# Performance work log

Hardware: AMD Instinct MI355X
Metric: run time of the kernel (lower is better)

The kernel has to match this reference:

```python
import jax, jax.numpy as jnp
import numpy as np

B, T, D = 4096, 200, 64
H = 32  # hidden units of score MLP
NEG_INF = jnp.float32(-2**32 + 1)


def setup_inputs() -> dict:
    key = jax.random.key(0)
    k1, k2, k3, k4, k5 = jax.random.split(key, 5)
    query = jax.random.normal(k1, (B, 1, D), dtype=jnp.float32)
    keys = jax.random.normal(k2, (B, T, D), dtype=jnp.float32)
    mask = jax.random.randint(k3, (B, T), 0, 2) > 0
    mask = mask.at[:, 0].set(True)  # ensure at least one valid key per row
    # Glorot-normal-ish init for the tiny score MLP
    W1 = jax.random.normal(k4, (3 * D, H), dtype=jnp.float32) * jnp.sqrt(2.0 / (3 * D + H))
    b1 = jnp.zeros((H,), dtype=jnp.float32)
    W2 = jax.random.normal(k5, (H, 1), dtype=jnp.float32) * jnp.sqrt(2.0 / (H + 1))
    b2 = jnp.zeros((1,), dtype=jnp.float32)
    return {"query": query, "keys": keys, "mask": mask,
            "W1": W1, "b1": b1, "W2": W2, "b2": b2}


def reference(query, keys, mask, W1, b1, W2, b2):
    b, t, d = keys.shape
    q = jnp.broadcast_to(query, (b, t, d))            # tile query over seq
    att_in = jnp.concatenate([q, keys, q - keys], axis=-1)   # [B,T,3D]
    h = jax.nn.sigmoid(att_in @ W1 + b1)              # [B,T,H]
    score = (h @ W2 + b2)[..., 0]                     # [B,T]
    score = jnp.where(mask, score, NEG_INF)
    w = jax.nn.softmax(score, axis=-1)                # [B,T]
    out = jnp.einsum('bt,btd->bd', w, keys)           # weighted key sum
    return out[:, None, :]                            # [B,1,D]
```

## Files before the change

kernel.cpp:

```cpp
#include <hip/hip_runtime.h>
#include <hip/hip_bf16.h>


#define B 4096
#define T 200
#define D 64
#define H 32
#define LOG2E 1.44269504088896340736f
#define SOFF 16.0f
#define NTILE 13

typedef __attribute__((ext_vector_type(8))) short short8;
typedef __attribute__((ext_vector_type(4))) float f32x4;


__global__ __launch_bounds__(256) void prep_kernel(
        const float* __restrict__ W1,
        const float* __restrict__ b1,
        const float* __restrict__ query,
        float*       __restrict__ ws)
{
    int blk = blockIdx.x;
    int tid = threadIdx.x;
    if (blk < 512) {
        int n = blk * 256 + tid;
        int b = n >> 5;
        int j = n & 31;
        const float* qb = query + (size_t)b * D;
        float acc = b1[j];
        #pragma unroll 8
        for (int i = 0; i < D; ++i)
            acc = fmaf(qb[i], W1[i * H + j] + W1[(128 + i) * H + j], acc);
        ws[n] = acc;
    } else {
        int m = (blk - 512) * 256 + tid;
        int e  = m & 7;
        int l  = (m >> 3) & 63;
        int fs = m >> 9;
        int ntile = fs >> 1, kstep = fs & 1;
        int k = kstep * 32 + (l >> 4) * 8 + e;
        int j = ntile * 16 + (l & 15);
        float v = W1[(64 + k) * H + j] - W1[(128 + k) * H + j];
        __hip_bfloat16 hv = __float2bfloat16(v);
        reinterpret_cast<unsigned short*>(ws + 131072)[m] =
            __builtin_bit_cast(unsigned short, hv);
    }
}

__device__ __forceinline__ unsigned short bf16u(float x) {
    __hip_bfloat16 h = __float2bfloat16(x);
    return __builtin_bit_cast(unsigned short, h);
}

__global__ __launch_bounds__(256) void attn_pool_kernel(
        const float* __restrict__ keys,
        const int*   __restrict__ mask,
        const unsigned short* __restrict__ wkf,
        const float* __restrict__ qa_all,
        const float* __restrict__ W2,
        float*       __restrict__ out)
{
    const int tid  = threadIdx.x;
    const int wv   = tid >> 6;
    const int lane = tid & 63;
    const int quad = lane >> 4;
    const int l15  = lane & 15;

    const int b = blockIdx.x * 4 + wv;

    const short8* wf = reinterpret_cast<const short8*>(wkf);
    short8 bf0 = wf[0 * 64 + lane];
    short8 bf1 = wf[1 * 64 + lane];
    short8 bf2 = wf[2 * 64 + lane];
    short8 bf3 = wf[3 * 64 + lane];

    const float* qa = qa_all + (size_t)b * H;
    const float qa0 = qa[l15];
    const float qa1 = qa[16 + l15];
    const float w20 = W2[l15];
    const float w21 = W2[16 + l15];

    const float4* krow = reinterpret_cast<const float4*>(keys + (size_t)b * (T * D));
    const int*    mrow = mask + (size_t)b * T;
    const int ib = quad * 2;

    float acc[16];
    #pragma unroll
    for (int j = 0; j < 16; ++j) acc[j] = 0.0f;
    float dacc = 0.0f;

    float4 kA0 = krow[l15 * 16 + ib + 0];
    float4 kA1 = krow[l15 * 16 + ib + 1];
    float4 kA2 = krow[l15 * 16 + 8 + ib + 0];
    float4 kA3 = krow[l15 * 16 + 8 + ib + 1];
    int    mA  = mrow[l15];

    #pragma unroll 1
    for (int tile = 0; tile < NTILE; ++tile) {
        float4 kB0 = kA0, kB1 = kA1, kB2 = kA2, kB3 = kA3;
        int    mB  = mA;
        if (tile + 1 < NTILE) {
            int tn  = (tile + 1) * 16 + l15;
            int trn = (tn < T) ? tn : (T - 1);
            kB0 = krow[trn * 16 + ib + 0];
            kB1 = krow[trn * 16 + ib + 1];
            kB2 = krow[trn * 16 + 8 + ib + 0];
            kB3 = krow[trn * 16 + 8 + ib + 1];
            mB  = mrow[trn];
        }

        short8 a0, a1;
        a0[0] = (short)bf16u(kA0.x); a0[1] = (short)bf16u(kA0.y);
        a0[2] = (short)bf16u(kA0.z); a0[3] = (short)bf16u(kA0.w);
        a0[4] = (short)bf16u(kA1.x); a0[5] = (short)bf16u(kA1.y);
        a0[6] = (short)bf16u(kA1.z); a0[7] = (short)bf16u(kA1.w);
        a1[0] = (short)bf16u(kA2.x); a1[1] = (short)bf16u(kA2.y);
        a1[2] = (short)bf16u(kA2.z); a1[3] = (short)bf16u(kA2.w);
        a1[4] = (short)bf16u(kA3.x); a1[5] = (short)bf16u(kA3.y);
        a1[6] = (short)bf16u(kA3.z); a1[7] = (short)bf16u(kA3.w);

        f32x4 c0 = {0.f, 0.f, 0.f, 0.f};
        f32x4 c1 = {0.f, 0.f, 0.f, 0.f};
        c0 = __builtin_amdgcn_mfma_f32_16x16x32_bf16(a0, bf0, c0, 0, 0, 0);
        c0 = __builtin_amdgcn_mfma_f32_16x16x32_bf16(a1, bf1, c0, 0, 0, 0);
        c1 = __builtin_amdgcn_mfma_f32_16x16x32_bf16(a0, bf2, c1, 0, 0, 0);
        c1 = __builtin_amdgcn_mfma_f32_16x16x32_bf16(a1, bf3, c1, 0, 0, 0);

        float p[4];
        #pragma unroll
        for (int r = 0; r < 4; ++r) {
            float x0 = c0[r] + qa0;
            float x1 = c1[r] + qa1;
            float s0 = __builtin_amdgcn_rcpf(1.0f + exp2f(-x0 * LOG2E));
            float s1 = __builtin_amdgcn_rcpf(1.0f + exp2f(-x1 * LOG2E));
            p[r] = fmaf(s0, w20, s1 * w21);
        }
        #pragma unroll
        for (int r = 0; r < 4; ++r) {
            #pragma unroll
            for (int off = 1; off <= 8; off <<= 1)
                p[r] += __shfl_xor(p[r], off, 64);
        }
        const int addr = (l15 >> 2) << 6;
        int q0 = __builtin_amdgcn_ds_bpermute(addr, __builtin_bit_cast(int, p[0]));
        int q1 = __builtin_amdgcn_ds_bpermute(addr, __builtin_bit_cast(int, p[1]));
        int q2 = __builtin_amdgcn_ds_bpermute(addr, __builtin_bit_cast(int, p[2]));
        int q3 = __builtin_amdgcn_ds_bpermute(addr, __builtin_bit_cast(int, p[3]));
        const int rsel = l15 & 3;
        int s01 = (rsel & 1) ? q1 : q0;
        int s23 = (rsel & 1) ? q3 : q2;
        float st = __builtin_bit_cast(float, (rsel & 2) ? s23 : s01);

        const int t = tile * 16 + l15;
        const float w = ((t < T) && (mA != 0)) ? exp2f((st - SOFF) * LOG2E) : 0.0f;

        acc[0]  = fmaf(w, kA0.x, acc[0]);  acc[1]  = fmaf(w, kA0.y, acc[1]);
        acc[2]  = fmaf(w, kA0.z, acc[2]);  acc[3]  = fmaf(w, kA0.w, acc[3]);
        acc[4]  = fmaf(w, kA1.x, acc[4]);  acc[5]  = fmaf(w, kA1.y, acc[5]);
        acc[6]  = fmaf(w, kA1.z, acc[6]);  acc[7]  = fmaf(w, kA1.w, acc[7]);
        acc[8]  = fmaf(w, kA2.x, acc[8]);  acc[9]  = fmaf(w, kA2.y, acc[9]);
        acc[10] = fmaf(w, kA2.z, acc[10]); acc[11] = fmaf(w, kA2.w, acc[11]);
        acc[12] = fmaf(w, kA3.x, acc[12]); acc[13] = fmaf(w, kA3.y, acc[13]);
        acc[14] = fmaf(w, kA3.z, acc[14]); acc[15] = fmaf(w, kA3.w, acc[15]);
        dacc += w;

        kA0 = kB0; kA1 = kB1; kA2 = kB2; kA3 = kB3; mA = mB;
    }

    #pragma unroll
    for (int j = 0; j < 16; ++j) {
        #pragma unroll
        for (int off = 1; off <= 8; off <<= 1)
            acc[j] += __shfl_xor(acc[j], off, 64);
    }
    #pragma unroll
    for (int off = 1; off <= 8; off <<= 1)
        dacc += __shfl_xor(dacc, off, 64);

    if (l15 == 0) {
        float rw = __builtin_amdgcn_rcpf(dacc);
        float4 o0 = {acc[0]  * rw, acc[1]  * rw, acc[2]  * rw, acc[3]  * rw};
        float4 o1 = {acc[4]  * rw, acc[5]  * rw, acc[6]  * rw, acc[7]  * rw};
        float4 o2 = {acc[8]  * rw, acc[9]  * rw, acc[10] * rw, acc[11] * rw};
        float4 o3 = {acc[12] * rw, acc[13] * rw, acc[14] * rw, acc[15] * rw};
        float4* ob = reinterpret_cast<float4*>(out + (size_t)b * D);
        ob[ib + 0]     = o0;
        ob[ib + 1]     = o1;
        ob[8 + ib + 0] = o2;
        ob[8 + ib + 1] = o3;
    }
}

extern "C" void kernel_launch(void* const* d_in, const int* in_sizes, int n_in,
                              void* d_out, int out_size, void* d_ws, size_t ws_size,
                              hipStream_t stream) {
    const float* query = (const float*)d_in[0];
    const float* keys  = (const float*)d_in[1];
    const int*   mask  = (const int*)d_in[2];
    const float* W1    = (const float*)d_in[3];
    const float* b1    = (const float*)d_in[4];
    const float* W2    = (const float*)d_in[5];

    float* ws = (float*)d_ws;
    float* qa = ws;
    unsigned short* wkf = (unsigned short*)(ws + 131072);

    prep_kernel<<<520, 256, 0, stream>>>(W1, b1, query, ws);
    attn_pool_kernel<<<B / 4, 256, 0, stream>>>(keys, mask, wkf, qa, W2,
                                                (float*)d_out);
}
```

Measured before the change: 310.3 us.

## Split each sequence across two waves and fold query projection into main kernel

The per-batch query projection (query·(W1a+W1c)+b1) moves out of the 512-block prep kernel and into the attention kernel. The prep kernel now only builds the summed weight matrix and the bf16 key-weight fragments. Each batch row's 200 keys are split across two wavefronts (7 and 6 tiles), which doubles the grid and halves each wave's serial loop. Partial sums and denominators are combined through shared memory behind a block barrier. The cost is extra in-kernel projection work per wave and a __syncthreads.

```diff
diff --git a/kernel.cpp b/kernel.cpp
--- a/kernel.cpp
+++ b/kernel.cpp
@@ -16,24 +16,15 @@
 
 __global__ __launch_bounds__(256) void prep_kernel(
         const float* __restrict__ W1,
-        const float* __restrict__ b1,
-        const float* __restrict__ query,
         float*       __restrict__ ws)
 {
-    int blk = blockIdx.x;
-    int tid = threadIdx.x;
-    if (blk < 512) {
-        int n = blk * 256 + tid;
-        int b = n >> 5;
+    int n = blockIdx.x * 256 + threadIdx.x;
+    if (blockIdx.x < 8) {
+        int k = n >> 5;
         int j = n & 31;
-        const float* qb = query + (size_t)b * D;
-        float acc = b1[j];
-        #pragma unroll 8
-        for (int i = 0; i < D; ++i)
-            acc = fmaf(qb[i], W1[i * H + j] + W1[(128 + i) * H + j], acc);
-        ws[n] = acc;
+        ws[n] = W1[k * H + j] + W1[(128 + k) * H + j];
     } else {
-        int m = (blk - 512) * 256 + tid;
+        int m = n - 2048;
         int e  = m & 7;
         int l  = (m >> 3) & 63;
         int fs = m >> 9;
@@ -42,7 +33,7 @@
         int j = ntile * 16 + (l & 15);
         float v = W1[(64 + k) * H + j] - W1[(128 + k) * H + j];
         __hip_bfloat16 hv = __float2bfloat16(v);
-        reinterpret_cast<unsigned short*>(ws + 131072)[m] =
+        reinterpret_cast<unsigned short*>(ws + 2048)[m] =
             __builtin_bit_cast(unsigned short, hv);
     }
 }
@@ -56,27 +47,45 @@
         const float* __restrict__ keys,
         const int*   __restrict__ mask,
         const unsigned short* __restrict__ wkf,
-        const float* __restrict__ qa_all,
+        const float* __restrict__ wsum,
+        const float* __restrict__ b1,
         const float* __restrict__ W2,
+        const float* __restrict__ query,
         float*       __restrict__ out)
 {
+    __shared__ float qsh[4][64];
+    __shared__ float part[4][68];
+
     const int tid  = threadIdx.x;
     const int wv   = tid >> 6;
     const int lane = tid & 63;
     const int quad = lane >> 4;
     const int l15  = lane & 15;
 
-    const int b = blockIdx.x * 4 + wv;
+    const int b    = blockIdx.x * 2 + (wv >> 1);
+    const int half = wv & 1;
+
+    qsh[wv][lane] = query[(size_t)b * D + lane];
+    const int jq = lane & 31;
+    const int kh = lane >> 5;
+    float qac0 = kh ? 0.0f : b1[jq];
+    float qac1 = 0.0f;
+    #pragma unroll
+    for (int k0 = 0; k0 < 32; k0 += 2) {
+        int k = kh * 32 + k0;
+        qac0 = fmaf(qsh[wv][k],     wsum[k * H + jq],       qac0);
+        qac1 = fmaf(qsh[wv][k + 1], wsum[(k + 1) * H + jq], qac1);
+    }
+    float qac = qac0 + qac1;
+    qac += __shfl_xor(qac, 32, 64);
+    const float qa0 = __shfl(qac, l15, 64);
+    const float qa1 = __shfl(qac, 16 + l15, 64);
 
     const short8* wf = reinterpret_cast<const short8*>(wkf);
     short8 bf0 = wf[0 * 64 + lane];
     short8 bf1 = wf[1 * 64 + lane];
     short8 bf2 = wf[2 * 64 + lane];
     short8 bf3 = wf[3 * 64 + lane];
-
-    const float* qa = qa_all + (size_t)b * H;
-    const float qa0 = qa[l15];
-    const float qa1 = qa[16 + l15];
     const float w20 = W2[l15];
     const float w21 = W2[16 + l15];
 
@@ -89,17 +98,21 @@
     for (int j = 0; j < 16; ++j) acc[j] = 0.0f;
     float dacc = 0.0f;
 
-    float4 kA0 = krow[l15 * 16 + ib + 0];
-    float4 kA1 = krow[l15 * 16 + ib + 1];
-    float4 kA2 = krow[l15 * 16 + 8 + ib + 0];
-    float4 kA3 = krow[l15 * 16 + 8 + ib + 1];
-    int    mA  = mrow[l15];
+    const int t0  = half * 7;
+    const int ntl = half ? 6 : 7;
+
+    float4 kA0 = krow[(t0 * 16 + l15) * 16 + ib + 0];
+    float4 kA1 = krow[(t0 * 16 + l15) * 16 + ib + 1];
+    float4 kA2 = krow[(t0 * 16 + l15) * 16 + 8 + ib + 0];
+    float4 kA3 = krow[(t0 * 16 + l15) * 16 + 8 + ib + 1];
+    int    mA  = mrow[t0 * 16 + l15];
 
     #pragma unroll 1
-    for (int tile = 0; tile < NTILE; ++tile) {
+    for (int it = 0; it < ntl; ++it) {
+        const int tile = t0 + it;
         float4 kB0 = kA0, kB1 = kA1, kB2 = kA2, kB3 = kA3;
         int    mB  = mA;
-        if (tile + 1 < NTILE) {
+        if (it + 1 < ntl) {
             int tn  = (tile + 1) * 16 + l15;
             int trn = (tn < T) ? tn : (T - 1);
             kB0 = krow[trn * 16 + ib + 0];
@@ -178,16 +191,24 @@
         dacc += __shfl_xor(dacc, off, 64);
 
     if (l15 == 0) {
-        float rw = __builtin_amdgcn_rcpf(dacc);
-        float4 o0 = {acc[0]  * rw, acc[1]  * rw, acc[2]  * rw, acc[3]  * rw};
-        float4 o1 = {acc[4]  * rw, acc[5]  * rw, acc[6]  * rw, acc[7]  * rw};
-        float4 o2 = {acc[8]  * rw, acc[9]  * rw, acc[10] * rw, acc[11] * rw};
-        float4 o3 = {acc[12] * rw, acc[13] * rw, acc[14] * rw, acc[15] * rw};
-        float4* ob = reinterpret_cast<float4*>(out + (size_t)b * D);
-        ob[ib + 0]     = o0;
-        ob[ib + 1]     = o1;
-        ob[8 + ib + 0] = o2;
-        ob[8 + ib + 1] = o3;
+        float4 o0 = {acc[0],  acc[1],  acc[2],  acc[3]};
+        float4 o1 = {acc[4],  acc[5],  acc[6],  acc[7]};
+        float4 o2 = {acc[8],  acc[9],  acc[10], acc[11]};
+        float4 o3 = {acc[12], acc[13], acc[14], acc[15]};
+        *reinterpret_cast<float4*>(&part[wv][quad * 8 + 0])      = o0;
+        *reinterpret_cast<float4*>(&part[wv][quad * 8 + 4])      = o1;
+        *reinterpret_cast<float4*>(&part[wv][32 + quad * 8 + 0]) = o2;
+        *reinterpret_cast<float4*>(&part[wv][32 + quad * 8 + 4]) = o3;
+    }
+    if (lane == 0) part[wv][64] = dacc;
+    __syncthreads();
+
+    if (tid < 128) {
+        int bb = tid >> 6;
+        int d  = tid & 63;
+        float s  = part[bb * 2][d]  + part[bb * 2 + 1][d];
+        float dn = part[bb * 2][64] + part[bb * 2 + 1][64];
+        out[((size_t)blockIdx.x * 2 + bb) * D + d] = s * __builtin_amdgcn_rcpf(dn);
     }
 }
 
@@ -202,10 +223,10 @@
     const float* W2    = (const float*)d_in[5];
 
     float* ws = (float*)d_ws;
-    float* qa = ws;
-    unsigned short* wkf = (unsigned short*)(ws + 131072);
-
-    prep_kernel<<<520, 256, 0, stream>>>(W1, b1, query, ws);
-    attn_pool_kernel<<<B / 4, 256, 0, stream>>>(keys, mask, wkf, qa, W2,
-                                                (float*)d_out);
-}
+    float* wsum = ws;
+    unsigned short* wkf = (unsigned short*)(ws + 2048);
+
+    prep_kernel<<<16, 256, 0, stream>>>(W1, ws);
+    attn_pool_kernel<<<B / 2, 256, 0, stream>>>(keys, mask, wkf, wsum, b1, W2,
+                                                query, (float*)d_out);
+}
```

Measured after the change: 303.8 us. 1.02x faster.
